# Kernel optimization log

Measured on AMD Instinct MI355X. Metric: run time of the kernel, lower is better.

The kernel has to match this reference:

```python
import jax, jax.numpy as jnp
import numpy as np

B, N, H, D = 2, 2048, 16, 128

def setup_inputs() -> dict:
    key = jax.random.key(0)
    kq, kk, kv = jax.random.split(key, 3)
    return {
        "query": jax.random.normal(kq, (B, N, H, D), dtype=jnp.float32),
        "key": jax.random.normal(kk, (B, N, H, D), dtype=jnp.float32),
        "value": jax.random.normal(kv, (B, N, H, D), dtype=jnp.float32),
    }

def reference(query, key, value):
    # inputs are [b, n, h, d]; module transposes to [b, h, n, d]
    q = jnp.transpose(query, (0, 2, 1, 3))  # bhnd
    k = jnp.transpose(key, (0, 2, 1, 3))    # bhmd
    v = jnp.transpose(value, (0, 2, 1, 3))  # bhmd
    # NOTE: original applies NO 1/sqrt(d) scaling
    scores = jnp.einsum('bhnd,bhmd->bhnm', q, k)
    attn = jax.nn.softmax(scores, axis=-1)
    return jnp.einsum('bhnm,bhmd->bhnd', attn, v)  # [b, h, n, d]
```

## Files before the change

### kernel.cpp

```cpp
#include <hip/hip_runtime.h>
#include <hip/hip_bf16.h>
#include <stdint.h>


constexpr int Bb = 2, Nn = 2048, Hh = 16, Dd = 128;
constexpr int ROWSTR = Hh * Dd;
constexpr size_t TEN = (size_t)Bb * Nn * Hh * Dd;
constexpr size_t WS_NEED = 2 * TEN * 2;

typedef __attribute__((ext_vector_type(8))) _Float16 f16x8;
typedef __attribute__((ext_vector_type(2))) __fp16 fp16x2;
typedef __attribute__((ext_vector_type(4))) float f32x4;
typedef __attribute__((ext_vector_type(16))) float f32x16;

__device__ __forceinline__ unsigned short f2h(float f) {
  union { _Float16 h; unsigned short u; } v;
  v.h = (_Float16)f;
  return v.u;
}

__device__ __forceinline__ unsigned pk2(float a, float b) {
  union { fp16x2 h; unsigned u; } v;
  v.h = __builtin_amdgcn_cvt_pkrtz(a, b);
  return v.u;
}

__device__ __forceinline__ void gload_lds16(const void* g, void* l) {
  __builtin_amdgcn_global_load_lds(
      (const __attribute__((address_space(1))) unsigned int*)g,
      (__attribute__((address_space(3))) unsigned int*)l, 16, 0, 0);
}

__device__ __forceinline__ f32x16 zero16() {
  f32x16 z;
#pragma unroll
  for (int i = 0; i < 16; ++i) z[i] = 0.f;
  return z;
}

__global__ __launch_bounds__(512) void conv_k(
    const float* __restrict__ K, _Float16* __restrict__ Kf) {
  size_t id = (size_t)blockIdx.x * 512 + threadIdx.x;
  size_t e = id * 8;
  float4 a = *(const float4*)(K + e);
  float4 b = *(const float4*)(K + e + 4);
  f16x8 t;
  t[0] = (_Float16)a.x; t[1] = (_Float16)a.y; t[2] = (_Float16)a.z; t[3] = (_Float16)a.w;
  t[4] = (_Float16)b.x; t[5] = (_Float16)b.y; t[6] = (_Float16)b.z; t[7] = (_Float16)b.w;
  *(f16x8*)(Kf + e) = t;
}

__global__ __launch_bounds__(256) void conv_v(
    const float* __restrict__ V, _Float16* __restrict__ Vt) {
  __shared__ alignas(16) short T[128 * 72];
  const int tid = threadIdx.x;
  const int bid = blockIdx.x;
  const int bh = bid >> 5;
  const int n0 = (bid & 31) * 64;
  const int h = bh & 15, b = bh >> 4;
  const float* src = V + (((size_t)b * Nn + n0) * Hh + h) * Dd;
#pragma unroll
  for (int it = 0; it < 8; ++it) {
    int id = it * 256 + tid;
    int f = id & 31, n = id >> 5;
    float4 a = *(const float4*)(src + (size_t)n * ROWSTR + f * 4);
    T[(4 * f + 0) * 72 + n] = (short)f2h(a.x);
    T[(4 * f + 1) * 72 + n] = (short)f2h(a.y);
    T[(4 * f + 2) * 72 + n] = (short)f2h(a.z);
    T[(4 * f + 3) * 72 + n] = (short)f2h(a.w);
  }
  __syncthreads();
  _Float16* dst = Vt + (size_t)bh * Dd * Nn + n0;
#pragma unroll
  for (int it = 0; it < 4; ++it) {
    int cid = it * 256 + tid;
    int d = cid >> 3, nc = cid & 7;
    f16x8 v = *(const f16x8*)((const char*)T + d * 144 + nc * 16);
    *(f16x8*)(dst + (size_t)d * Nn + nc * 8) = v;
  }
}

__global__ __launch_bounds__(256, 2) void attn32(
    const float* __restrict__ Q, const _Float16* __restrict__ Kf,
    const _Float16* __restrict__ Vt, float* __restrict__ O) {
  __shared__ alignas(16) char base[65536];

  const int tid = threadIdx.x;
  const int wave = tid >> 6;
  const int lane = tid & 63;
  const int l31 = lane & 31;
  const int hi = lane >> 5;

  const int raw = blockIdx.x;
  const int wg = (raw & 7) * 64 + (raw >> 3);
  const int qb = wg & 15;
  const int bh = wg >> 4;
  const int h = bh & 15, b = bh >> 4;

  const char* K0 = (const char*)Kf + ((size_t)b * Nn * Hh + h) * 256;
  const char* V0 = (const char*)Vt + (size_t)bh * Dd * Nn * 2;
  const float* Q0 = Q + ((size_t)b * Nn * Hh + h) * 128;
  float* Ob = O + (size_t)bh * Nn * Dd;

  const int wq0 = qb * 128 + wave * 32;
  const int kswz = (l31 & 15) << 4;
  const int vswz = (l31 & 7) << 4;

  auto STAGE = [&](int buf, int kt) {
    const size_t kv0 = (size_t)kt * 64;
    char* kd = base + buf * 16384;
    char* vd = base + 32768 + buf * 16384;
    const char* ks = K0 + kv0 * 4096;
    const char* vs = V0 + kv0 * 2;
#pragma unroll
    for (int i = 0; i < 4; ++i) {
      int ob = i * 4096 + wave * 1024;
      int o = ob + lane * 16;
      int kv = o >> 8, ck = o & 255;
      gload_lds16(ks + (size_t)kv * 4096 + (ck ^ ((kv & 15) << 4)), kd + ob);
      int d = o >> 7, cv = o & 127;
      gload_lds16(vs + (size_t)d * 4096 + (cv ^ ((d & 7) << 4)), vd + ob);
    }
  };

  STAGE(0, 0);

  f16x8 qf[8];
  {
    const float* qp = Q0 + (size_t)(wq0 + l31) * ROWSTR;
#pragma unroll
    for (int c = 0; c < 8; ++c) {
      const float* p = qp + c * 16 + hi * 8;
      float4 a = *(const float4*)p;
      float4 bb = *(const float4*)(p + 4);
      f16x8 t;
      t[0] = (_Float16)a.x;  t[1] = (_Float16)a.y;
      t[2] = (_Float16)a.z;  t[3] = (_Float16)a.w;
      t[4] = (_Float16)bb.x; t[5] = (_Float16)bb.y;
      t[6] = (_Float16)bb.z; t[7] = (_Float16)bb.w;
      qf[c] = t;
    }
  }

  f32x16 acc[4];
#pragma unroll
  for (int dt = 0; dt < 4; ++dt) acc[dt] = zero16();
  float m_run = -INFINITY, l_run = 0.f;

  __syncthreads();
  int cur = 0;

  for (int kt = 0; kt < Nn / 64; ++kt) {
    if (kt < Nn / 64 - 1) STAGE(cur ^ 1, kt + 1);
    const char* KB = base + cur * 16384;
    const char* VB = base + 32768 + cur * 16384;

    f32x16 s[2];
    s[0] = zero16();
    s[1] = zero16();
#pragma unroll
    for (int c = 0; c < 8; ++c) {
      const int colc = 32 * c + 16 * hi;
      f16x8 k0 = *(const f16x8*)(KB + l31 * 256 + (colc ^ kswz));
      f16x8 k1 = *(const f16x8*)(KB + (l31 + 32) * 256 + (colc ^ kswz));
      s[0] = __builtin_amdgcn_mfma_f32_32x32x16_f16(k0, qf[c], s[0], 0, 0, 0);
      s[1] = __builtin_amdgcn_mfma_f32_32x32x16_f16(k1, qf[c], s[1], 0, 0, 0);
    }

    float mx = s[0][0];
#pragma unroll
    for (int r = 1; r < 16; ++r) mx = fmaxf(mx, s[0][r]);
#pragma unroll
    for (int r = 0; r < 16; ++r) mx = fmaxf(mx, s[1][r]);
    mx = fmaxf(mx, __shfl_xor(mx, 32));

    if (!__all(mx <= m_run + 8.0f)) {
      float mn = fmaxf(m_run, mx);
      float e = exp2f((m_run - mn) * 1.44269504f);
      l_run *= e;
#pragma unroll
      for (int dt = 0; dt < 4; ++dt)
#pragma unroll
        for (int r = 0; r < 16; ++r) acc[dt][r] *= e;
      m_run = mn;
    }
    float ps = 0.f;
#pragma unroll
    for (int sub = 0; sub < 2; ++sub)
#pragma unroll
      for (int r = 0; r < 16; ++r) {
        float pv = exp2f((s[sub][r] - m_run) * 1.44269504f);
        s[sub][r] = pv;
        ps += pv;
      }
    ps += __shfl_xor(ps, 32);
    l_run += ps;

    f16x8 pa[4];
#pragma unroll
    for (int ks = 0; ks < 4; ++ks) {
      const int sub = ks >> 1, kb = ks & 1;
      float v0 = s[sub][8 * kb + 0], v1 = s[sub][8 * kb + 1];
      float v2 = s[sub][8 * kb + 2], v3 = s[sub][8 * kb + 3];
      float v4 = s[sub][8 * kb + 4], v5 = s[sub][8 * kb + 5];
      float v6 = s[sub][8 * kb + 6], v7 = s[sub][8 * kb + 7];
      unsigned uA0 = pk2(v0, v1), uA1 = pk2(v2, v3);
      unsigned uB0 = pk2(v4, v5), uB1 = pk2(v6, v7);
      unsigned r0 = (unsigned)__shfl_xor((int)(hi ? uA0 : uB0), 32);
      unsigned r1 = (unsigned)__shfl_xor((int)(hi ? uA1 : uB1), 32);
      union { unsigned u[4]; f16x8 v; } t;
      t.u[0] = hi ? r0 : uA0;
      t.u[1] = hi ? r1 : uA1;
      t.u[2] = hi ? uB0 : r0;
      t.u[3] = hi ? uB1 : r1;
      pa[ks] = t.v;
    }

#pragma unroll
    for (int dt = 0; dt < 4; ++dt) {
      const char* vrow = VB + (32 * dt + l31) * 128;
#pragma unroll
      for (int ks = 0; ks < 4; ++ks) {
        f16x8 vf = *(const f16x8*)(vrow + ((32 * ks + 16 * hi) ^ vswz));
        acc[dt] = __builtin_amdgcn_mfma_f32_32x32x16_f16(vf, pa[ks], acc[dt], 0, 0, 0);
      }
    }

    __syncthreads();
    cur ^= 1;
  }

  const float invl = 1.0f / l_run;
  float* orow = Ob + (size_t)(wq0 + l31) * Dd;
#pragma unroll
  for (int dt = 0; dt < 4; ++dt)
#pragma unroll
    for (int r = 0; r < 16; ++r) {
      int d = 32 * dt + (r & 3) + 8 * (r >> 2) + 4 * hi;
      orow[d] = acc[dt][r] * invl;
    }
}

__global__ __launch_bounds__(256, 2) void attn_fwd_kernel(
    const float* __restrict__ Q, const float* __restrict__ K,
    const float* __restrict__ V, float* __restrict__ O) {
  __shared__ alignas(16) short Klds[64 * Dd];
  __shared__ alignas(16) short Vtlds[Dd * 64];
  __shared__ alignas(16) short Plds[4][16 * 64];

  const int tid = threadIdx.x;
  const int wave = tid >> 6;
  const int lane = tid & 63;
  const int g = lane >> 4;
  const int l15 = lane & 15;

  const int qb = blockIdx.x & 31;
  const int h = (blockIdx.x >> 5) & 15;
  const int b = blockIdx.x >> 9;

  const float* Qb = Q + ((size_t)b * Nn * Hh + h) * Dd;
  const float* Kb = K + ((size_t)b * Nn * Hh + h) * Dd;
  const float* Vb = V + ((size_t)b * Nn * Hh + h) * Dd;
  float* Ob = O + ((size_t)(b * Hh + h) * Nn) * Dd;

  const int qrow = qb * 64 + wave * 16 + l15;
  f16x8 qf[4];
  {
    const float* qp = Qb + (size_t)qrow * ROWSTR;
#pragma unroll
    for (int c = 0; c < 4; ++c) {
      const float* p = qp + c * 32 + g * 8;
      float4 a = *(const float4*)(p);
      float4 bb = *(const float4*)(p + 4);
      f16x8 t;
      t[0] = (_Float16)a.x;  t[1] = (_Float16)a.y;
      t[2] = (_Float16)a.z;  t[3] = (_Float16)a.w;
      t[4] = (_Float16)bb.x; t[5] = (_Float16)bb.y;
      t[6] = (_Float16)bb.z; t[7] = (_Float16)bb.w;
      qf[c] = t;
    }
  }

  f32x4 acc[8];
#pragma unroll
  for (int i = 0; i < 8; ++i) acc[i] = (f32x4){0.f, 0.f, 0.f, 0.f};
  float m_run[4], l_run[4];
#pragma unroll
  for (int r = 0; r < 4; ++r) { m_run[r] = -INFINITY; l_run[r] = 0.f; }

  char* KB = (char*)Klds;
  char* VB = (char*)Vtlds;
  char* PB = (char*)(Plds[wave]);

  for (int kt = 0; kt < Nn / 64; ++kt) {
    const int kv0 = kt * 64;
    __syncthreads();
#pragma unroll
    for (int i = 0; i < 8; ++i) {
      int id = i * 256 + tid;
      int f = id & 31;
      int kv = id >> 5;
      const float* p = Kb + (size_t)(kv0 + kv) * ROWSTR + f * 4;
      float4 a = *(const float4*)p;
      unsigned long long pk =
          (unsigned long long)f2h(a.x) | ((unsigned long long)f2h(a.y) << 16) |
          ((unsigned long long)f2h(a.z) << 32) | ((unsigned long long)f2h(a.w) << 48);
      int byte = kv * 256 + ((f * 8) ^ ((kv & 7) << 4));
      *(unsigned long long*)(KB + byte) = pk;
    }
#pragma unroll
    for (int i = 0; i < 8; ++i) {
      int id = i * 256 + tid;
      int d = id & 127;
      int kq = id >> 7;
      const float* p = Vb + (size_t)(kv0 + kq * 4) * ROWSTR + d;
      float v0 = p[0];
      float v1 = p[ROWSTR];
      float v2 = p[2 * ROWSTR];
      float v3 = p[3 * ROWSTR];
      unsigned long long pk =
          (unsigned long long)f2h(v0) | ((unsigned long long)f2h(v1) << 16) |
          ((unsigned long long)f2h(v2) << 32) | ((unsigned long long)f2h(v3) << 48);
      int byte = d * 128 + ((kq * 8) ^ ((d & 7) << 4));
      *(unsigned long long*)(VB + byte) = pk;
    }
    __syncthreads();

    f32x4 s[4];
#pragma unroll
    for (int t = 0; t < 4; ++t) {
      f32x4 cacc = (f32x4){0.f, 0.f, 0.f, 0.f};
      int row = t * 16 + l15;
#pragma unroll
      for (int c = 0; c < 4; ++c) {
        int byte = row * 256 + (((c * 64) + g * 16) ^ ((row & 7) << 4));
        f16x8 kf = *(const f16x8*)(KB + byte);
        cacc = __builtin_amdgcn_mfma_f32_16x16x32_f16(qf[c], kf, cacc, 0, 0, 0);
      }
      s[t] = cacc;
    }

#pragma unroll
    for (int r = 0; r < 4; ++r) {
      float mx = fmaxf(fmaxf(s[0][r], s[1][r]), fmaxf(s[2][r], s[3][r]));
      mx = fmaxf(mx, __shfl_xor(mx, 1));
      mx = fmaxf(mx, __shfl_xor(mx, 2));
      mx = fmaxf(mx, __shfl_xor(mx, 4));
      mx = fmaxf(mx, __shfl_xor(mx, 8));
      float mn = fmaxf(m_run[r], mx);
      float e = exp2f((m_run[r] - mn) * 1.44269504f);
      float ps = 0.f;
#pragma unroll
      for (int t = 0; t < 4; ++t) {
        float pv = exp2f((s[t][r] - mn) * 1.44269504f);
        s[t][r] = pv;
        ps += pv;
      }
      ps += __shfl_xor(ps, 1);
      ps += __shfl_xor(ps, 2);
      ps += __shfl_xor(ps, 4);
      ps += __shfl_xor(ps, 8);
      l_run[r] = l_run[r] * e + ps;
      m_run[r] = mn;
#pragma unroll
      for (int dt = 0; dt < 8; ++dt) acc[dt][r] *= e;
    }

#pragma unroll
    for (int t = 0; t < 4; ++t)
#pragma unroll
      for (int r = 0; r < 4; ++r) {
        int q = g * 4 + r;
        int kv = t * 16 + l15;
        int byte = q * 128 + ((kv * 2) ^ ((q & 7) << 4));
        *(unsigned short*)(PB + byte) = f2h(s[t][r]);
      }

#pragma unroll
    for (int c2 = 0; c2 < 2; ++c2) {
      int pbyte = l15 * 128 + (((c2 * 64) + g * 16) ^ ((l15 & 7) << 4));
      f16x8 pf = *(const f16x8*)(PB + pbyte);
#pragma unroll
      for (int dt = 0; dt < 8; ++dt) {
        int d = dt * 16 + l15;
        int vbyte = d * 128 + (((c2 * 64) + g * 16) ^ ((d & 7) << 4));
        f16x8 vf = *(const f16x8*)(VB + vbyte);
        acc[dt] = __builtin_amdgcn_mfma_f32_16x16x32_f16(pf, vf, acc[dt], 0, 0, 0);
      }
    }
  }

  const int qout = qb * 64 + wave * 16;
#pragma unroll
  for (int r = 0; r < 4; ++r) {
    float inv = 1.0f / l_run[r];
    float* op = Ob + (size_t)(qout + g * 4 + r) * Dd + l15;
#pragma unroll
    for (int dt = 0; dt < 8; ++dt) {
      op[dt * 16] = acc[dt][r] * inv;
    }
  }
}

extern "C" void kernel_launch(void* const* d_in, const int* in_sizes, int n_in,
                              void* d_out, int out_size, void* d_ws, size_t ws_size,
                              hipStream_t stream) {
  const float* Q = (const float*)d_in[0];
  const float* K = (const float*)d_in[1];
  const float* V = (const float*)d_in[2];
  float* O = (float*)d_out;

  if (ws_size >= WS_NEED) {
    _Float16* Kf = (_Float16*)d_ws;
    _Float16* Vt = Kf + TEN;
    conv_k<<<dim3(TEN / 8 / 512), 512, 0, stream>>>(K, Kf);
    conv_v<<<dim3(1024), 256, 0, stream>>>(V, Vt);
    attn32<<<dim3(512), 256, 0, stream>>>(Q, Kf, Vt, O);
  } else {
    attn_fwd_kernel<<<dim3(1024), 256, 0, stream>>>(Q, K, V, O);
  }
}
```

Before: 222.0 us.

## Software-pipeline QK of next tile with softmax/PV of current; merge conversion kernels

Restructures the attention main loop so the QK^T MFMAs for tile k+1 are issued before the softmax and PV of tile k. K and V staging are split and skewed to match, and the loop is unrolled by two with ping-pong score registers. It also adds s_setprio around the MFMA blocks, uses a tree max reduction and split partial sums. Separately, the K and V fp16 conversion kernels are fused into one launch to save a kernel launch. The cost is more live score registers, which risks spills or lower occupancy.

```diff
diff --git a/kernel.cpp b/kernel.cpp
--- a/kernel.cpp
+++ b/kernel.cpp
@@ -38,45 +38,46 @@
   return z;
 }
 
-__global__ __launch_bounds__(512) void conv_k(
-    const float* __restrict__ K, _Float16* __restrict__ Kf) {
-  size_t id = (size_t)blockIdx.x * 512 + threadIdx.x;
-  size_t e = id * 8;
-  float4 a = *(const float4*)(K + e);
-  float4 b = *(const float4*)(K + e + 4);
-  f16x8 t;
-  t[0] = (_Float16)a.x; t[1] = (_Float16)a.y; t[2] = (_Float16)a.z; t[3] = (_Float16)a.w;
-  t[4] = (_Float16)b.x; t[5] = (_Float16)b.y; t[6] = (_Float16)b.z; t[7] = (_Float16)b.w;
-  *(f16x8*)(Kf + e) = t;
-}
-
-__global__ __launch_bounds__(256) void conv_v(
-    const float* __restrict__ V, _Float16* __restrict__ Vt) {
-  __shared__ alignas(16) short T[128 * 72];
-  const int tid = threadIdx.x;
+__global__ __launch_bounds__(256) void conv_kv(
+    const float* __restrict__ K, const float* __restrict__ V,
+    _Float16* __restrict__ Kf, _Float16* __restrict__ Vt) {
   const int bid = blockIdx.x;
-  const int bh = bid >> 5;
-  const int n0 = (bid & 31) * 64;
-  const int h = bh & 15, b = bh >> 4;
-  const float* src = V + (((size_t)b * Nn + n0) * Hh + h) * Dd;
-#pragma unroll
-  for (int it = 0; it < 8; ++it) {
-    int id = it * 256 + tid;
-    int f = id & 31, n = id >> 5;
-    float4 a = *(const float4*)(src + (size_t)n * ROWSTR + f * 4);
-    T[(4 * f + 0) * 72 + n] = (short)f2h(a.x);
-    T[(4 * f + 1) * 72 + n] = (short)f2h(a.y);
-    T[(4 * f + 2) * 72 + n] = (short)f2h(a.z);
-    T[(4 * f + 3) * 72 + n] = (short)f2h(a.w);
-  }
-  __syncthreads();
-  _Float16* dst = Vt + (size_t)bh * Dd * Nn + n0;
-#pragma unroll
-  for (int it = 0; it < 4; ++it) {
-    int cid = it * 256 + tid;
-    int d = cid >> 3, nc = cid & 7;
-    f16x8 v = *(const f16x8*)((const char*)T + d * 144 + nc * 16);
-    *(f16x8*)(dst + (size_t)d * Nn + nc * 8) = v;
+  if (bid < 4096) {
+    size_t id = (size_t)bid * 256 + threadIdx.x;
+    size_t e = id * 8;
+    float4 a = *(const float4*)(K + e);
+    float4 b = *(const float4*)(K + e + 4);
+    f16x8 t;
+    t[0] = (_Float16)a.x; t[1] = (_Float16)a.y; t[2] = (_Float16)a.z; t[3] = (_Float16)a.w;
+    t[4] = (_Float16)b.x; t[5] = (_Float16)b.y; t[6] = (_Float16)b.z; t[7] = (_Float16)b.w;
+    *(f16x8*)(Kf + e) = t;
+  } else {
+    __shared__ alignas(16) short T[128 * 72];
+    const int tid = threadIdx.x;
+    const int vb = bid - 4096;
+    const int bh = vb >> 5;
+    const int n0 = (vb & 31) * 64;
+    const int h = bh & 15, b = bh >> 4;
+    const float* src = V + (((size_t)b * Nn + n0) * Hh + h) * Dd;
+#pragma unroll
+    for (int it = 0; it < 8; ++it) {
+      int id = it * 256 + tid;
+      int f = id & 31, n = id >> 5;
+      float4 a = *(const float4*)(src + (size_t)n * ROWSTR + f * 4);
+      T[(4 * f + 0) * 72 + n] = (short)f2h(a.x);
+      T[(4 * f + 1) * 72 + n] = (short)f2h(a.y);
+      T[(4 * f + 2) * 72 + n] = (short)f2h(a.z);
+      T[(4 * f + 3) * 72 + n] = (short)f2h(a.w);
+    }
+    __syncthreads();
+    _Float16* dst = Vt + (size_t)bh * Dd * Nn + n0;
+#pragma unroll
+    for (int it = 0; it < 4; ++it) {
+      int cid = it * 256 + tid;
+      int d = cid >> 3, nc = cid & 7;
+      f16x8 v = *(const f16x8*)((const char*)T + d * 144 + nc * 16);
+      *(f16x8*)(dst + (size_t)d * Nn + nc * 8) = v;
+    }
   }
 }
 
@@ -106,24 +107,116 @@
   const int kswz = (l31 & 15) << 4;
   const int vswz = (l31 & 7) << 4;
 
-  auto STAGE = [&](int buf, int kt) {
-    const size_t kv0 = (size_t)kt * 64;
-    char* kd = base + buf * 16384;
-    char* vd = base + 32768 + buf * 16384;
-    const char* ks = K0 + kv0 * 4096;
-    const char* vs = V0 + kv0 * 2;
-#pragma unroll
-    for (int i = 0; i < 4; ++i) {
-      int ob = i * 4096 + wave * 1024;
-      int o = ob + lane * 16;
-      int kv = o >> 8, ck = o & 255;
-      gload_lds16(ks + (size_t)kv * 4096 + (ck ^ ((kv & 15) << 4)), kd + ob);
-      int d = o >> 7, cv = o & 127;
-      gload_lds16(vs + (size_t)d * 4096 + (cv ^ ((d & 7) << 4)), vd + ob);
-    }
-  };
-
-  STAGE(0, 0);
+#define STAGE_K(BUF, KT)                                                         \
+  do {                                                                           \
+    const char* ks_ = K0 + (size_t)(KT) * 64 * 4096;                             \
+    char* kd_ = base + (BUF) * 16384;                                            \
+    _Pragma("unroll") for (int i_ = 0; i_ < 4; ++i_) {                           \
+      int ob_ = i_ * 4096 + wave * 1024;                                         \
+      int o_ = ob_ + lane * 16;                                                  \
+      int kv_ = o_ >> 8, ck_ = o_ & 255;                                         \
+      gload_lds16(ks_ + (size_t)kv_ * 4096 + (ck_ ^ ((kv_ & 15) << 4)), kd_ + ob_); \
+    }                                                                            \
+  } while (0)
+
+#define STAGE_V(BUF, KT)                                                         \
+  do {                                                                           \
+    const char* vs_ = V0 + (size_t)(KT) * 64 * 2;                                \
+    char* vd_ = base + 32768 + (BUF) * 16384;                                    \
+    _Pragma("unroll") for (int i_ = 0; i_ < 4; ++i_) {                           \
+      int ob_ = i_ * 4096 + wave * 1024;                                         \
+      int o_ = ob_ + lane * 16;                                                  \
+      int d_ = o_ >> 7, cv_ = o_ & 127;                                          \
+      gload_lds16(vs_ + (size_t)d_ * 4096 + (cv_ ^ ((d_ & 7) << 4)), vd_ + ob_); \
+    }                                                                            \
+  } while (0)
+
+#define QK_TILE(BUF, S0, S1)                                                     \
+  do {                                                                           \
+    const char* KB_ = base + (BUF) * 16384;                                      \
+    S0 = zero16();                                                               \
+    S1 = zero16();                                                               \
+    __builtin_amdgcn_s_setprio(1);                                               \
+    _Pragma("unroll") for (int c_ = 0; c_ < 8; ++c_) {                           \
+      const int colc_ = 32 * c_ + 16 * hi;                                       \
+      f16x8 k0_ = *(const f16x8*)(KB_ + l31 * 256 + (colc_ ^ kswz));             \
+      f16x8 k1_ = *(const f16x8*)(KB_ + (l31 + 32) * 256 + (colc_ ^ kswz));      \
+      S0 = __builtin_amdgcn_mfma_f32_32x32x16_f16(k0_, qf[c_], S0, 0, 0, 0);     \
+      S1 = __builtin_amdgcn_mfma_f32_32x32x16_f16(k1_, qf[c_], S1, 0, 0, 0);     \
+    }                                                                            \
+    __builtin_amdgcn_s_setprio(0);                                               \
+  } while (0)
+
+#define PACK1(SRC, KB_IDX, KSIDX)                                                \
+  do {                                                                           \
+    float v0_ = SRC[8 * (KB_IDX) + 0], v1_ = SRC[8 * (KB_IDX) + 1];              \
+    float v2_ = SRC[8 * (KB_IDX) + 2], v3_ = SRC[8 * (KB_IDX) + 3];              \
+    float v4_ = SRC[8 * (KB_IDX) + 4], v5_ = SRC[8 * (KB_IDX) + 5];              \
+    float v6_ = SRC[8 * (KB_IDX) + 6], v7_ = SRC[8 * (KB_IDX) + 7];              \
+    unsigned uA0_ = pk2(v0_, v1_), uA1_ = pk2(v2_, v3_);                         \
+    unsigned uB0_ = pk2(v4_, v5_), uB1_ = pk2(v6_, v7_);                         \
+    unsigned r0_ = (unsigned)__shfl_xor((int)(hi ? uA0_ : uB0_), 32);            \
+    unsigned r1_ = (unsigned)__shfl_xor((int)(hi ? uA1_ : uB1_), 32);            \
+    union { unsigned u[4]; f16x8 v; } t2_;                                       \
+    t2_.u[0] = hi ? r0_ : uA0_;                                                  \
+    t2_.u[1] = hi ? r1_ : uA1_;                                                  \
+    t2_.u[2] = hi ? uB0_ : r0_;                                                  \
+    t2_.u[3] = hi ? uB1_ : r1_;                                                  \
+    pa_[KSIDX] = t2_.v;                                                          \
+  } while (0)
+
+#define SMAX_PV(P0, P1, VBUF)                                                    \
+  do {                                                                           \
+    const char* VB_ = base + 32768 + (VBUF) * 16384;                             \
+    float t_[16];                                                                \
+    _Pragma("unroll") for (int r_ = 0; r_ < 16; ++r_)                            \
+        t_[r_] = fmaxf(P0[r_], P1[r_]);                                          \
+    _Pragma("unroll") for (int w_ = 8; w_ >= 1; w_ >>= 1) {                      \
+      _Pragma("unroll") for (int r_ = 0; r_ < w_; ++r_)                          \
+          t_[r_] = fmaxf(t_[r_], t_[r_ + w_]);                                   \
+    }                                                                            \
+    float mx_ = fmaxf(t_[0], __shfl_xor(t_[0], 32));                             \
+    if (!__all(mx_ <= m_run + 8.0f)) {                                           \
+      float mn_ = fmaxf(m_run, mx_);                                             \
+      float e_ = exp2f((m_run - mn_) * 1.44269504f);                             \
+      l_run *= e_;                                                               \
+      _Pragma("unroll") for (int dt_ = 0; dt_ < 4; ++dt_) {                      \
+        _Pragma("unroll") for (int r_ = 0; r_ < 16; ++r_) acc[dt_][r_] *= e_;    \
+      }                                                                          \
+      m_run = mn_;                                                               \
+    }                                                                            \
+    float psA_[4] = {0.f, 0.f, 0.f, 0.f};                                        \
+    _Pragma("unroll") for (int r_ = 0; r_ < 16; ++r_) {                          \
+      float pv_ = exp2f((P0[r_] - m_run) * 1.44269504f);                         \
+      P0[r_] = pv_;                                                              \
+      psA_[r_ & 3] += pv_;                                                       \
+    }                                                                            \
+    _Pragma("unroll") for (int r_ = 0; r_ < 16; ++r_) {                          \
+      float pv_ = exp2f((P1[r_] - m_run) * 1.44269504f);                         \
+      P1[r_] = pv_;                                                              \
+      psA_[r_ & 3] += pv_;                                                       \
+    }                                                                            \
+    float ps_ = (psA_[0] + psA_[1]) + (psA_[2] + psA_[3]);                       \
+    ps_ += __shfl_xor(ps_, 32);                                                  \
+    l_run += ps_;                                                                \
+    f16x8 pa_[4];                                                                \
+    PACK1(P0, 0, 0);                                                             \
+    PACK1(P0, 1, 1);                                                             \
+    PACK1(P1, 0, 2);                                                             \
+    PACK1(P1, 1, 3);                                                             \
+    __builtin_amdgcn_s_setprio(1);                                               \
+    _Pragma("unroll") for (int dt_ = 0; dt_ < 4; ++dt_) {                        \
+      const char* vrow_ = VB_ + (32 * dt_ + l31) * 128;                          \
+      _Pragma("unroll") for (int ks_ = 0; ks_ < 4; ++ks_) {                      \
+        f16x8 vf_ = *(const f16x8*)(vrow_ + ((32 * ks_ + 16 * hi) ^ vswz));      \
+        acc[dt_] = __builtin_amdgcn_mfma_f32_32x32x16_f16(vf_, pa_[ks_],         \
+                                                          acc[dt_], 0, 0, 0);   \
+      }                                                                          \
+    }                                                                            \
+    __builtin_amdgcn_s_setprio(0);                                               \
+  } while (0)
+
+  STAGE_K(0, 0);
 
   f16x8 qf[8];
   {
@@ -147,88 +240,31 @@
   for (int dt = 0; dt < 4; ++dt) acc[dt] = zero16();
   float m_run = -INFINITY, l_run = 0.f;
 
+  f32x16 sA0, sA1, sB0, sB1;
+
   __syncthreads();
-  int cur = 0;
-
-  for (int kt = 0; kt < Nn / 64; ++kt) {
-    if (kt < Nn / 64 - 1) STAGE(cur ^ 1, kt + 1);
-    const char* KB = base + cur * 16384;
-    const char* VB = base + 32768 + cur * 16384;
-
-    f32x16 s[2];
-    s[0] = zero16();
-    s[1] = zero16();
-#pragma unroll
-    for (int c = 0; c < 8; ++c) {
-      const int colc = 32 * c + 16 * hi;
-      f16x8 k0 = *(const f16x8*)(KB + l31 * 256 + (colc ^ kswz));
-      f16x8 k1 = *(const f16x8*)(KB + (l31 + 32) * 256 + (colc ^ kswz));
-      s[0] = __builtin_amdgcn_mfma_f32_32x32x16_f16(k0, qf[c], s[0], 0, 0, 0);
-      s[1] = __builtin_amdgcn_mfma_f32_32x32x16_f16(k1, qf[c], s[1], 0, 0, 0);
-    }
-
-    float mx = s[0][0];
-#pragma unroll
-    for (int r = 1; r < 16; ++r) mx = fmaxf(mx, s[0][r]);
-#pragma unroll
-    for (int r = 0; r < 16; ++r) mx = fmaxf(mx, s[1][r]);
-    mx = fmaxf(mx, __shfl_xor(mx, 32));
-
-    if (!__all(mx <= m_run + 8.0f)) {
-      float mn = fmaxf(m_run, mx);
-      float e = exp2f((m_run - mn) * 1.44269504f);
-      l_run *= e;
-#pragma unroll
-      for (int dt = 0; dt < 4; ++dt)
-#pragma unroll
-        for (int r = 0; r < 16; ++r) acc[dt][r] *= e;
-      m_run = mn;
-    }
-    float ps = 0.f;
-#pragma unroll
-    for (int sub = 0; sub < 2; ++sub)
-#pragma unroll
-      for (int r = 0; r < 16; ++r) {
-        float pv = exp2f((s[sub][r] - m_run) * 1.44269504f);
-        s[sub][r] = pv;
-        ps += pv;
-      }
-    ps += __shfl_xor(ps, 32);
-    l_run += ps;
-
-    f16x8 pa[4];
-#pragma unroll
-    for (int ks = 0; ks < 4; ++ks) {
-      const int sub = ks >> 1, kb = ks & 1;
-      float v0 = s[sub][8 * kb + 0], v1 = s[sub][8 * kb + 1];
-      float v2 = s[sub][8 * kb + 2], v3 = s[sub][8 * kb + 3];
-      float v4 = s[sub][8 * kb + 4], v5 = s[sub][8 * kb + 5];
-      float v6 = s[sub][8 * kb + 6], v7 = s[sub][8 * kb + 7];
-      unsigned uA0 = pk2(v0, v1), uA1 = pk2(v2, v3);
-      unsigned uB0 = pk2(v4, v5), uB1 = pk2(v6, v7);
-      unsigned r0 = (unsigned)__shfl_xor((int)(hi ? uA0 : uB0), 32);
-      unsigned r1 = (unsigned)__shfl_xor((int)(hi ? uA1 : uB1), 32);
-      union { unsigned u[4]; f16x8 v; } t;
-      t.u[0] = hi ? r0 : uA0;
-      t.u[1] = hi ? r1 : uA1;
-      t.u[2] = hi ? uB0 : r0;
-      t.u[3] = hi ? uB1 : r1;
-      pa[ks] = t.v;
-    }
-
-#pragma unroll
-    for (int dt = 0; dt < 4; ++dt) {
-      const char* vrow = VB + (32 * dt + l31) * 128;
-#pragma unroll
-      for (int ks = 0; ks < 4; ++ks) {
-        f16x8 vf = *(const f16x8*)(vrow + ((32 * ks + 16 * hi) ^ vswz));
-        acc[dt] = __builtin_amdgcn_mfma_f32_32x32x16_f16(vf, pa[ks], acc[dt], 0, 0, 0);
-      }
-    }
-
+  STAGE_K(1, 1);
+  STAGE_V(0, 0);
+  QK_TILE(0, sA0, sA1);
+  __syncthreads();
+
+  for (int kt = 1; kt < 31; kt += 2) {
+    STAGE_K((kt + 1) & 1, kt + 1);
+    STAGE_V(kt & 1, kt);
+    QK_TILE(kt & 1, sB0, sB1);
+    SMAX_PV(sA0, sA1, 0);
     __syncthreads();
-    cur ^= 1;
-  }
+    STAGE_K((kt + 2) & 1, kt + 2);
+    STAGE_V((kt + 1) & 1, kt + 1);
+    QK_TILE((kt + 1) & 1, sA0, sA1);
+    SMAX_PV(sB0, sB1, 1);
+    __syncthreads();
+  }
+  STAGE_V(1, 31);
+  QK_TILE(1, sB0, sB1);
+  SMAX_PV(sA0, sA1, 0);
+  __syncthreads();
+  SMAX_PV(sB0, sB1, 1);
 
   const float invl = 1.0f / l_run;
   float* orow = Ob + (size_t)(wq0 + l31) * Dd;
@@ -239,6 +275,12 @@
       int d = 32 * dt + (r & 3) + 8 * (r >> 2) + 4 * hi;
       orow[d] = acc[dt][r] * invl;
     }
+
+#undef STAGE_K
+#undef STAGE_V
+#undef QK_TILE
+#undef PACK1
+#undef SMAX_PV
 }
 
 __global__ __launch_bounds__(256, 2) void attn_fwd_kernel(
@@ -413,8 +455,7 @@
   if (ws_size >= WS_NEED) {
     _Float16* Kf = (_Float16*)d_ws;
     _Float16* Vt = Kf + TEN;
-    conv_k<<<dim3(TEN / 8 / 512), 512, 0, stream>>>(K, Kf);
-    conv_v<<<dim3(1024), 256, 0, stream>>>(V, Vt);
+    conv_kv<<<dim3(5120), 256, 0, stream>>>(K, V, Kf, Vt);
     attn32<<<dim3(512), 256, 0, stream>>>(Q, Kf, Vt, O);
   } else {
     attn_fwd_kernel<<<dim3(1024), 256, 0, stream>>>(Q, K, V, O);
```

After: 231.3 us. 4.2% more time.
